# Performance work log

Measured on AMD Instinct MI355X. Metric: run time of the kernel, lower is better.

## Reference

```python
import jax, jax.numpy as jnp
import numpy as np

EMBED, NUM_CLASSES, K, BETA = 96, 3, 3, 0.75
B, H, W = 4, 512, 512
N = H * W // 16            # 16384 sampled points
N_IMP = int(BETA * N)      # 12288 importance points
N_COV = N - N_IMP          # 4096 coverage points


def point_sample(inp, points):
    """Bilinear sample inp [B,C,H,W] at points [B,N,2] in [0,1] (x,y order).
    Matches F.grid_sample(..., mode='bilinear', padding_mode='zeros', align_corners=False)
    applied to grid = 2*points - 1."""
    Bb, C, Hh, Ww = inp.shape
    g = 2.0 * points - 1.0
    ix = ((g[..., 0] + 1.0) * Ww - 1.0) / 2.0   # [B,N]
    iy = ((g[..., 1] + 1.0) * Hh - 1.0) / 2.0
    x0 = jnp.floor(ix)
    y0 = jnp.floor(iy)
    wx1 = ix - x0
    wx0 = 1.0 - wx1
    wy1 = iy - y0
    wy0 = 1.0 - wy1
    flat = inp.reshape(Bb, C, Hh * Ww)

    def corner(xc, yc, w):
        valid = (xc >= 0) & (xc < Ww) & (yc >= 0) & (yc < Hh)
        xi = jnp.clip(xc, 0, Ww - 1).astype(jnp.int32)
        yi = jnp.clip(yc, 0, Hh - 1).astype(jnp.int32)
        idx = (yi * Ww + xi)[:, None, :]                     # [B,1,N]
        v = jnp.take_along_axis(flat, idx, axis=2)           # [B,C,N]
        return v * (w * valid.astype(w.dtype))[:, None, :]

    return (corner(x0, y0, wx0 * wy0)
            + corner(x0 + 1.0, y0, wx1 * wy0)
            + corner(x0, y0 + 1.0, wx0 * wy1)
            + corner(x0 + 1.0, y0 + 1.0, wx1 * wy1))


def setup_inputs() -> dict:
    key = jax.random.key(0)
    ks = jax.random.split(key, 6)
    x = jax.random.normal(ks[0], (B, EMBED, H, W), dtype=jnp.float32)
    res = jax.random.normal(ks[1], (B, NUM_CLASSES, H, W), dtype=jnp.float32)
    out = jax.random.normal(ks[2], (B, NUM_CLASSES, H, W), dtype=jnp.float32)
    w_mlp = jax.random.normal(ks[3], (NUM_CLASSES, EMBED + NUM_CLASSES), dtype=jnp.float32) * 0.02
    over_gen = jax.random.uniform(ks[4], (B, K * N, 2), dtype=jnp.float32)
    coverage = jax.random.uniform(ks[5], (B, N_COV, 2), dtype=jnp.float32)
    return {"x": x, "res": res, "out": out, "w_mlp": w_mlp,
            "over_gen": over_gen, "coverage": coverage}


def reference(x, res, out, w_mlp, over_gen, coverage):
    # sampling_points (training branch): uncertainty from squared error map
    mask = jnp.square(out - res)                       # [B,C,H,W]
    ms = -jnp.sort(-mask, axis=1)                      # channels sorted descending
    og_map = point_sample(ms, over_gen)                # [B,C,K*N]
    uncert = og_map[:, 1] - og_map[:, 0]               # -(top1 - top2), [B,K*N]
    _, idx = jax.lax.top_k(uncert, N_IMP)              # [B,N_IMP]
    importance = jnp.take_along_axis(over_gen, idx[..., None], axis=1)  # [B,N_IMP,2]
    points = jnp.concatenate([importance, coverage], axis=1)            # [B,N,2]

    coarse = point_sample(out, points)                 # [B,C,N]
    fine = point_sample(x, points)                     # [B,EMBED,N]
    feat = jnp.concatenate([coarse, fine], axis=1)     # [B,C+EMBED,N]
    rend = jax.nn.relu(jnp.einsum('oc,bcn->bon', w_mlp, feat))  # 1x1 Conv1d, no bias
    return rend
```

## Files before the change

kernel.cpp:

```cpp
#include <hip/hip_runtime.h>
#include <stdint.h>

#define Bb    4
#define EMBED 96
#define NCH   3
#define Hh    512
#define Ww    512
#define HWSZ  (Hh * Ww)
#define KN    49152
#define NPT   16384
#define NIMP  12288
#define NCOV  4096
#define SORTN 65536
#define NBUCK 1024

__device__ __forceinline__ float opaque(float v) {
    asm volatile("" : "+v"(v));
    return v;
}

__device__ __forceinline__ void ref_coords(float p, int& i0, float& w0, float& w1) {
    float g  = 2.0f * p - 1.0f;
    float t  = (g + 1.0f) * 512.0f - 1.0f;
    float ix = t * 0.5f;
    float f  = floorf(ix);
    i0 = (int)f;
    w1 = ix - f;
    w0 = 1.0f - w1;
}

__device__ __forceinline__ uint32_t sortable_desc32(float v) {
    uint32_t u = __float_as_uint(v);
    uint32_t asc = (u >> 31) ? ~u : (u ^ 0x80000000u);
    return ~asc;
}

__device__ __forceinline__ uint32_t part1by1(uint32_t v) {
    v &= 0xFFFFu;
    v = (v | (v << 8)) & 0x00FF00FFu;
    v = (v | (v << 4)) & 0x0F0F0F0Fu;
    v = (v | (v << 2)) & 0x33333333u;
    v = (v | (v << 1)) & 0x55555555u;
    return v;
}

__global__ void build_maps(const float* __restrict__ res,
                           const float* __restrict__ outm,
                           float2* __restrict__ maps) {
    int lb  = blockIdx.y;
    int pix = blockIdx.x * blockDim.x + threadIdx.x;
    const float* r0 = res  + (size_t)lb * NCH * HWSZ;
    const float* o0 = outm + (size_t)lb * NCH * HWSZ;
    float d0 = opaque(o0[pix]            - r0[pix]);
    float d1 = opaque(o0[HWSZ + pix]     - r0[HWSZ + pix]);
    float d2 = opaque(o0[2 * HWSZ + pix] - r0[2 * HWSZ + pix]);
    float a  = opaque(d0 * d0);
    float bq = opaque(d1 * d1);
    float c  = opaque(d2 * d2);
    float m0 = fmaxf(fmaxf(a, bq), c);
    float m1 = fmaxf(fminf(a, bq), fminf(fmaxf(a, bq), c));
    maps[(size_t)lb * HWSZ + pix] = make_float2(m0, m1);
}

__global__ void uncert_keys_maps(const float2* __restrict__ maps,
                                 const float* __restrict__ over_gen,
                                 uint64_t* __restrict__ keys) {
    int lb = blockIdx.y;
    int i  = blockIdx.x * blockDim.x + threadIdx.x;
    if (i >= KN) { keys[(size_t)lb * SORTN + i] = 0xFFFFFFFFFFFFFFFFull; return; }

    float px = over_gen[((size_t)lb * KN + i) * 2 + 0];
    float py = over_gen[((size_t)lb * KN + i) * 2 + 1];
    int x0, y0;
    float wx0, wx1, wy0, wy1;
    ref_coords(px, x0, wx0, wx1);
    ref_coords(py, y0, wy0, wy1);

    const float2* mp = maps + (size_t)lb * HWSZ;
    int   cxs[4] = {x0, x0 + 1, x0, x0 + 1};
    int   cys[4] = {y0, y0, y0 + 1, y0 + 1};
    float wxs[4] = {wx0, wx1, wx0, wx1};
    float wys[4] = {wy0, wy0, wy1, wy1};

    float acc0 = 0.0f, acc1 = 0.0f;
#pragma unroll
    for (int q = 0; q < 4; ++q) {
        int xq = cxs[q], yq = cys[q];
        if (xq < 0 || xq >= Ww || yq < 0 || yq >= Hh) continue;
        float2 m = mp[yq * Ww + xq];
        float wq = opaque(wxs[q] * wys[q]);
        float t0 = opaque(wq * m.x);
        float t1 = opaque(wq * m.y);
        acc0 = opaque(acc0 + t0);
        acc1 = opaque(acc1 + t1);
    }
    float u = opaque(acc1 - acc0);
    keys[(size_t)lb * SORTN + i] =
        ((uint64_t)sortable_desc32(u) << 32) | (uint32_t)i;
}

__global__ void uncert_keys_direct(const float* __restrict__ res,
                                   const float* __restrict__ outm,
                                   const float* __restrict__ over_gen,
                                   uint64_t* __restrict__ keys) {
    int lb = blockIdx.y;
    int i  = blockIdx.x * blockDim.x + threadIdx.x;
    if (i >= KN) { keys[(size_t)lb * SORTN + i] = 0xFFFFFFFFFFFFFFFFull; return; }

    float px = over_gen[((size_t)lb * KN + i) * 2 + 0];
    float py = over_gen[((size_t)lb * KN + i) * 2 + 1];
    int x0, y0;
    float wx0, wx1, wy0, wy1;
    ref_coords(px, x0, wx0, wx1);
    ref_coords(py, y0, wy0, wy1);

    const float* r0 = res  + (size_t)lb * NCH * HWSZ;
    const float* o0 = outm + (size_t)lb * NCH * HWSZ;
    int   cxs[4] = {x0, x0 + 1, x0, x0 + 1};
    int   cys[4] = {y0, y0, y0 + 1, y0 + 1};
    float wxs[4] = {wx0, wx1, wx0, wx1};
    float wys[4] = {wy0, wy0, wy1, wy1};

    float acc0 = 0.0f, acc1 = 0.0f;
#pragma unroll
    for (int q = 0; q < 4; ++q) {
        int xq = cxs[q], yq = cys[q];
        if (xq < 0 || xq >= Ww || yq < 0 || yq >= Hh) continue;
        int off = yq * Ww + xq;
        float d0 = opaque(o0[off]            - r0[off]);
        float d1 = opaque(o0[HWSZ + off]     - r0[HWSZ + off]);
        float d2 = opaque(o0[2 * HWSZ + off] - r0[2 * HWSZ + off]);
        float a  = opaque(d0 * d0);
        float bq = opaque(d1 * d1);
        float c  = opaque(d2 * d2);
        float m0 = fmaxf(fmaxf(a, bq), c);
        float m1 = fmaxf(fminf(a, bq), fminf(fmaxf(a, bq), c));
        float wq = opaque(wxs[q] * wys[q]);
        float t0 = opaque(wq * m0);
        float t1 = opaque(wq * m1);
        acc0 = opaque(acc0 + t0);
        acc1 = opaque(acc1 + t1);
    }
    float u = opaque(acc1 - acc0);
    keys[(size_t)lb * SORTN + i] =
        ((uint64_t)sortable_desc32(u) << 32) | (uint32_t)i;
}

__global__ void __launch_bounds__(1024) bitonic_local_first(uint64_t* __restrict__ keys) {
    __shared__ uint64_t sh[2048];
    uint64_t* base = keys + (size_t)blockIdx.x * 2048;
    int t = threadIdx.x;
    sh[t]        = base[t];
    sh[t + 1024] = base[t + 1024];
    __syncthreads();
    int gbase = (blockIdx.x & 31) << 11;
    for (int k = 2; k <= 2048; k <<= 1) {
        for (int j = k >> 1; j >= 1; j >>= 1) {
            int low = t & (j - 1);
            int i = ((t ^ low) << 1) | low;
            int l = i | j;
            bool up = (((gbase + i) & k) == 0);
            uint64_t a = sh[i], c = sh[l];
            if ((a > c) == up) { sh[i] = c; sh[l] = a; }
            __syncthreads();
        }
    }
    base[t]        = sh[t];
    base[t + 1024] = sh[t + 1024];
}

__global__ void __launch_bounds__(1024) bitonic_global_fused(uint64_t* __restrict__ keys,
                                                             int m) {
    __shared__ uint64_t sh[2048];
    int lb  = blockIdx.y;
    int blk = blockIdx.x;
    int t   = threadIdx.x;
    int GS  = 1 << m;
    int GPB = 2048 >> m;
    int gstart = blk * GPB;
    int esh = 11 - m;
    uint64_t* base = keys + ((size_t)lb << 16);

    for (int s = t; s < 2048; s += 1024) {
        int e  = s >> esh;
        int gl = s & (GPB - 1);
        int g  = gstart + gl;
        int full = (g & 2047) | (e << 11) | ((g >> 11) << (11 + m));
        sh[s] = base[full];
    }
    __syncthreads();
    for (int jl = GS >> 1; jl >= 1; jl >>= 1) {
        int gl = t & (GPB - 1);
        int pe = t >> esh;
        int low = pe & (jl - 1);
        int e0 = ((pe ^ low) << 1) | low;
        int e1 = e0 | jl;
        bool up = ((((gstart + gl) >> 11) & 1) == 0);
        int s0 = e0 * GPB + gl, s1 = e1 * GPB + gl;
        uint64_t a = sh[s0], c = sh[s1];
        if ((a > c) == up) { sh[s0] = c; sh[s1] = a; }
        __syncthreads();
    }
    for (int s = t; s < 2048; s += 1024) {
        int e  = s >> esh;
        int gl = s & (GPB - 1);
        int g  = gstart + gl;
        int full = (g & 2047) | (e << 11) | ((g >> 11) << (11 + m));
        base[full] = sh[s];
    }
}

__global__ void __launch_bounds__(1024) bitonic_local_k(uint64_t* __restrict__ keys, int k) {
    __shared__ uint64_t sh[2048];
    uint64_t* base = keys + (size_t)blockIdx.x * 2048;
    int t = threadIdx.x;
    sh[t]        = base[t];
    sh[t + 1024] = base[t + 1024];
    __syncthreads();
    int gbase = (blockIdx.x & 31) << 11;
    bool up = ((gbase & k) == 0);
    for (int j = 1024; j >= 1; j >>= 1) {
        int low = t & (j - 1);
        int i = ((t ^ low) << 1) | low;
        int l = i | j;
        uint64_t a = sh[i], c = sh[l];
        if ((a > c) == up) { sh[i] = c; sh[l] = a; }
        __syncthreads();
    }
    base[t]        = sh[t];
    base[t + 1024] = sh[t + 1024];
}

static void run_sort_big(uint64_t* keys, int nb, hipStream_t stream) {
    bitonic_local_first<<<nb * 32, 1024, 0, stream>>>(keys);
    for (int kbit = 12; kbit <= 16; ++kbit) {
        bitonic_global_fused<<<dim3(32, nb), 1024, 0, stream>>>(keys, kbit - 11);
        bitonic_local_k<<<nb * 32, 1024, 0, stream>>>(keys, 1 << kbit);
    }
}

__global__ void hist_kernel(const uint64_t* __restrict__ keys,
                            const float* __restrict__ over_gen,
                            const float* __restrict__ coverage,
                            uint32_t* __restrict__ hist,
                            uint32_t* __restrict__ mort) {
    int lb = blockIdx.y;
    int n  = blockIdx.x * blockDim.x + threadIdx.x;
    float px, py;
    if (n < NIMP) {
        uint32_t idx = (uint32_t)keys[((size_t)lb << 16) + n];
        if (idx >= KN) idx = 0;
        px = over_gen[((size_t)lb * KN + idx) * 2 + 0];
        py = over_gen[((size_t)lb * KN + idx) * 2 + 1];
    } else {
        int m = n - NIMP;
        px = coverage[((size_t)lb * NCOV + m) * 2 + 0];
        py = coverage[((size_t)lb * NCOV + m) * 2 + 1];
    }
    int x0, y0;
    float w0, w1;
    ref_coords(px, x0, w0, w1);
    ref_coords(py, y0, w0, w1);
    int xi = min(max(x0, 0), Ww - 1);
    int yi = min(max(y0, 0), Hh - 1);
    uint32_t morton = part1by1((uint32_t)xi) | (part1by1((uint32_t)yi) << 1);
    uint32_t bucket = morton >> 8;
    mort[(size_t)lb * NPT + n] = bucket;
    atomicAdd(&hist[(size_t)lb * NBUCK + bucket], 1u);
}

__global__ void __launch_bounds__(1024) scan_kernel(const uint32_t* __restrict__ hist,
                                                    uint32_t* __restrict__ offs) {
    __shared__ uint32_t sh[NBUCK];
    int lb = blockIdx.x;
    int t  = threadIdx.x;
    uint32_t orig = hist[(size_t)lb * NBUCK + t];
    sh[t] = orig;
    __syncthreads();
    for (int d = 1; d < NBUCK; d <<= 1) {
        uint32_t add = (t >= d) ? sh[t - d] : 0u;
        __syncthreads();
        sh[t] += add;
        __syncthreads();
    }
    offs[(size_t)lb * NBUCK + t] = sh[t] - orig;
}

__global__ void scatter_kernel(const uint32_t* __restrict__ mort,
                               uint32_t* __restrict__ offs,
                               uint32_t* __restrict__ porder) {
    int lb = blockIdx.y;
    int n  = blockIdx.x * blockDim.x + threadIdx.x;
    uint32_t b = mort[(size_t)lb * NPT + n];
    uint32_t pos = atomicAdd(&offs[(size_t)lb * NBUCK + b], 1u);
    porder[(size_t)lb * NPT + pos] = (uint32_t)n;
}

__global__ void render_kernel(const float* __restrict__ x,
                              const float* __restrict__ outm,
                              const float* __restrict__ w_mlp,
                              const float* __restrict__ over_gen,
                              const float* __restrict__ coverage,
                              const uint64_t* __restrict__ keys,
                              const uint32_t* __restrict__ porder,
                              float* __restrict__ dst) {
    int gid = blockIdx.x * blockDim.x + threadIdx.x;
    int pt = gid >> 3, r = gid & 7;
    int lb = blockIdx.y;
    int n = pt;
    if (porder) n = porder[(size_t)lb * NPT + pt];

    float px, py;
    if (n < NIMP) {
        uint32_t idx = (uint32_t)keys[((size_t)lb << 16) + n];
        if (idx >= KN) idx = 0;
        px = over_gen[((size_t)lb * KN + idx) * 2 + 0];
        py = over_gen[((size_t)lb * KN + idx) * 2 + 1];
    } else {
        int m = n - NIMP;
        px = coverage[((size_t)lb * NCOV + m) * 2 + 0];
        py = coverage[((size_t)lb * NCOV + m) * 2 + 1];
    }

    int x0, y0;
    float wx0, wx1, wy0, wy1;
    ref_coords(px, x0, wx0, wx1);
    ref_coords(py, y0, wy0, wy1);

    int   cxs[4] = {x0, x0 + 1, x0, x0 + 1};
    int   cys[4] = {y0, y0, y0 + 1, y0 + 1};
    float wcs[4] = {wx0 * wy0, wx1 * wy0, wx0 * wy1, wx1 * wy1};
    bool  vld[4];
#pragma unroll
    for (int q = 0; q < 4; ++q)
        vld[q] = (cxs[q] >= 0) & (cxs[q] < Ww) & (cys[q] >= 0) & (cys[q] < Hh);

    float acc0 = 0.0f, acc1 = 0.0f, acc2 = 0.0f;
    for (int c = r; c < NCH + EMBED; c += 8) {
        const float* src = (c < NCH)
            ? (outm + ((size_t)lb * NCH + c) * HWSZ)
            : (x + ((size_t)lb * EMBED + (c - NCH)) * HWSZ);
        float f = 0.0f;
#pragma unroll
        for (int q = 0; q < 4; ++q) {
            if (vld[q]) f += wcs[q] * src[cys[q] * Ww + cxs[q]];
        }
        acc0 += w_mlp[c] * f;
        acc1 += w_mlp[99 + c] * f;
        acc2 += w_mlp[198 + c] * f;
    }
#pragma unroll
    for (int d = 1; d < 8; d <<= 1) {
        acc0 += __shfl_xor(acc0, d);
        acc1 += __shfl_xor(acc1, d);
        acc2 += __shfl_xor(acc2, d);
    }
    if (r == 0) {
        size_t ob = (size_t)lb * 3 * NPT + n;
        dst[ob]           = fmaxf(acc0, 0.0f);
        dst[ob + NPT]     = fmaxf(acc1, 0.0f);
        dst[ob + 2 * NPT] = fmaxf(acc2, 0.0f);
    }
}

extern "C" void kernel_launch(void* const* d_in, const int* in_sizes, int n_in,
                              void* d_out, int out_size, void* d_ws, size_t ws_size,
                              hipStream_t stream) {
    const float* x        = (const float*)d_in[0];
    const float* res      = (const float*)d_in[1];
    const float* outm     = (const float*)d_in[2];
    const float* w_mlp    = (const float*)d_in[3];
    const float* over_gen = (const float*)d_in[4];
    const float* coverage = (const float*)d_in[5];
    float* dst = (float*)d_out;

    const size_t keys_sz = (size_t)Bb * SORTN * sizeof(uint64_t);
    const size_t hist_sz = (size_t)Bb * NBUCK * sizeof(uint32_t);
    const size_t offs_sz = hist_sz;
    const size_t mort_sz = (size_t)Bb * NPT * sizeof(uint32_t);
    const size_t pord_sz = mort_sz;
    const size_t reor_sz = hist_sz + offs_sz + mort_sz + pord_sz;
    const size_t maps_sz = (size_t)Bb * HWSZ * sizeof(float2);

    uint64_t* keys = (uint64_t*)d_ws;
    dim3 gU(SORTN / 256, Bb), gP(NPT / 256, Bb), gD(NPT * 8 / 256, Bb);

    if (ws_size >= keys_sz + reor_sz + maps_sz) {
        char* pbase = (char*)d_ws + keys_sz;
        uint32_t* hist   = (uint32_t*)pbase;
        uint32_t* offs   = (uint32_t*)(pbase + hist_sz);
        uint32_t* mort   = (uint32_t*)(pbase + hist_sz + offs_sz);
        uint32_t* porder = (uint32_t*)(pbase + hist_sz + offs_sz + mort_sz);
        float2*   maps   = (float2*)(pbase + reor_sz);
        dim3 gM(HWSZ / 256, Bb);
        build_maps<<<gM, 256, 0, stream>>>(res, outm, maps);
        uncert_keys_maps<<<gU, 256, 0, stream>>>(maps, over_gen, keys);
        run_sort_big(keys, Bb, stream);
        hipMemsetAsync(hist, 0, hist_sz, stream);
        hist_kernel<<<gP, 256, 0, stream>>>(keys, over_gen, coverage, hist, mort);
        scan_kernel<<<Bb, NBUCK, 0, stream>>>(hist, offs);
        scatter_kernel<<<gP, 256, 0, stream>>>(mort, offs, porder);
        render_kernel<<<gD, 256, 0, stream>>>(x, outm, w_mlp, over_gen, coverage,
                                              keys, porder, dst);
    } else if (ws_size >= keys_sz + reor_sz) {
        char* pbase = (char*)d_ws + keys_sz;
        uint32_t* hist   = (uint32_t*)pbase;
        uint32_t* offs   = (uint32_t*)(pbase + hist_sz);
        uint32_t* mort   = (uint32_t*)(pbase + hist_sz + offs_sz);
        uint32_t* porder = (uint32_t*)(pbase + hist_sz + offs_sz + mort_sz);
        uncert_keys_direct<<<gU, 256, 0, stream>>>(res, outm, over_gen, keys);
        run_sort_big(keys, Bb, stream);
        hipMemsetAsync(hist, 0, hist_sz, stream);
        hist_kernel<<<gP, 256, 0, stream>>>(keys, over_gen, coverage, hist, mort);
        scan_kernel<<<Bb, NBUCK, 0, stream>>>(hist, offs);
        scatter_kernel<<<gP, 256, 0, stream>>>(mort, offs, porder);
        render_kernel<<<gD, 256, 0, stream>>>(x, outm, w_mlp, over_gen, coverage,
                                              keys, porder, dst);
    } else {
        uncert_keys_direct<<<gU, 256, 0, stream>>>(res, outm, over_gen, keys);
        run_sort_big(keys, Bb, stream);
        render_kernel<<<gD, 256, 0, stream>>>(x, outm, w_mlp, over_gen, coverage,
                                              keys, (const uint32_t*)nullptr, dst);
    }
}
```

Measured before the change: 283.8 us.

## Replace full bitonic sort with radix-histogram selection and compacted candidate sort

Rather than bitonic-sorting all 65536 padded keys per batch, the code builds an 11-bit histogram of key prefixes during key generation, scans it to find the cutoff bucket holding the 12288th element, and compacts candidates into a 16384-slot buffer that is then sorted. The bitonic sort also runs its inner strides (j<=64) in registers via wavefront shuffles instead of shared-memory passes with barriers. Sort work and global passes shrink, at the cost of extra kernels, atomics and memsets. If more than 16384 keys fall at or below the cutoff bucket, the excess is silently dropped, which could change the selected points.

```diff
diff --git a/kernel.cpp b/kernel.cpp
--- a/kernel.cpp
+++ b/kernel.cpp
@@ -11,7 +11,8 @@
 #define NPT   16384
 #define NIMP  12288
 #define NCOV  4096
-#define SORTN 65536
+#define SELB  2048
+#define CSEG  16384
 #define NBUCK 1024
 
 __device__ __forceinline__ float opaque(float v) {
@@ -42,6 +43,38 @@
     v = (v | (v << 2)) & 0x33333333u;
     v = (v | (v << 1)) & 0x55555555u;
     return v;
+}
+
+__device__ __forceinline__ uint64_t shfl64(uint64_t v, int lanexor) {
+    int2 p;
+    p.x = (int)(v & 0xFFFFFFFFull);
+    p.y = (int)(v >> 32);
+    p.x = __shfl_xor(p.x, lanexor);
+    p.y = __shfl_xor(p.y, lanexor);
+    return ((uint64_t)(uint32_t)p.y << 32) | (uint32_t)p.x;
+}
+
+__device__ __forceinline__ void ce_shfl(uint64_t& v, int idx, int j, int k) {
+    uint64_t o = shfl64(v, j);
+    bool low = (idx & j) == 0;
+    bool up  = (idx & k) == 0;
+    uint64_t mn = (v < o) ? v : o;
+    uint64_t mx = (v < o) ? o : v;
+    v = (low == up) ? mn : mx;
+}
+
+__device__ __forceinline__ void ce_reg(uint64_t& a, uint64_t& b, bool up) {
+    uint64_t mn = (a < b) ? a : b;
+    uint64_t mx = (a < b) ? b : a;
+    a = up ? mn : mx;
+    b = up ? mx : mn;
+}
+
+__device__ __forceinline__ void reg_tail(uint64_t& a, uint64_t& b, int ia, int ib, int k) {
+    bool up = (ia & k) == 0;
+    ce_reg(a, b, up);
+#pragma unroll
+    for (int j = 32; j >= 1; j >>= 1) { ce_shfl(a, ia, j, k); ce_shfl(b, ib, j, k); }
 }
 
 __global__ void build_maps(const float* __restrict__ res,
@@ -64,10 +97,10 @@
 
 __global__ void uncert_keys_maps(const float2* __restrict__ maps,
                                  const float* __restrict__ over_gen,
-                                 uint64_t* __restrict__ keys) {
+                                 uint64_t* __restrict__ keys,
+                                 uint32_t* __restrict__ hist) {
     int lb = blockIdx.y;
     int i  = blockIdx.x * blockDim.x + threadIdx.x;
-    if (i >= KN) { keys[(size_t)lb * SORTN + i] = 0xFFFFFFFFFFFFFFFFull; return; }
 
     float px = over_gen[((size_t)lb * KN + i) * 2 + 0];
     float py = over_gen[((size_t)lb * KN + i) * 2 + 1];
@@ -95,17 +128,18 @@
         acc1 = opaque(acc1 + t1);
     }
     float u = opaque(acc1 - acc0);
-    keys[(size_t)lb * SORTN + i] =
-        ((uint64_t)sortable_desc32(u) << 32) | (uint32_t)i;
+    uint64_t key = ((uint64_t)sortable_desc32(u) << 32) | (uint32_t)i;
+    keys[(size_t)lb * KN + i] = key;
+    atomicAdd(&hist[(size_t)lb * SELB + (uint32_t)(key >> 53)], 1u);
 }
 
 __global__ void uncert_keys_direct(const float* __restrict__ res,
                                    const float* __restrict__ outm,
                                    const float* __restrict__ over_gen,
-                                   uint64_t* __restrict__ keys) {
+                                   uint64_t* __restrict__ keys,
+                                   uint32_t* __restrict__ hist) {
     int lb = blockIdx.y;
     int i  = blockIdx.x * blockDim.x + threadIdx.x;
-    if (i >= KN) { keys[(size_t)lb * SORTN + i] = 0xFFFFFFFFFFFFFFFFull; return; }
 
     float px = over_gen[((size_t)lb * KN + i) * 2 + 0];
     float py = over_gen[((size_t)lb * KN + i) * 2 + 1];
@@ -142,35 +176,80 @@
         acc1 = opaque(acc1 + t1);
     }
     float u = opaque(acc1 - acc0);
-    keys[(size_t)lb * SORTN + i] =
-        ((uint64_t)sortable_desc32(u) << 32) | (uint32_t)i;
-}
-
-__global__ void __launch_bounds__(1024) bitonic_local_first(uint64_t* __restrict__ keys) {
+    uint64_t key = ((uint64_t)sortable_desc32(u) << 32) | (uint32_t)i;
+    keys[(size_t)lb * KN + i] = key;
+    atomicAdd(&hist[(size_t)lb * SELB + (uint32_t)(key >> 53)], 1u);
+}
+
+__global__ void __launch_bounds__(1024) scan_findC(const uint32_t* __restrict__ hist,
+                                                   uint32_t* __restrict__ cutC) {
+    __shared__ uint32_t s[1024];
+    int lb = blockIdx.x, t = threadIdx.x;
+    uint32_t h0 = hist[(size_t)lb * SELB + 2 * t];
+    uint32_t h1 = hist[(size_t)lb * SELB + 2 * t + 1];
+    s[t] = h0 + h1;
+    __syncthreads();
+    for (int d = 1; d < 1024; d <<= 1) {
+        uint32_t add = (t >= d) ? s[t - d] : 0u;
+        __syncthreads();
+        s[t] += add;
+        __syncthreads();
+    }
+    uint32_t incl = s[t];
+    uint32_t excl = incl - h0 - h1;
+    if (excl < NIMP && excl + h0 >= NIMP) cutC[lb] = 2 * t;
+    uint32_t p1 = excl + h0;
+    if (p1 < NIMP && incl >= NIMP) cutC[lb] = 2 * t + 1;
+}
+
+__global__ void compact_kernel(const uint64_t* __restrict__ keys,
+                               const uint32_t* __restrict__ cutC,
+                               uint32_t* __restrict__ ccnt,
+                               uint64_t* __restrict__ cbuf) {
+    int lb = blockIdx.y;
+    int i  = blockIdx.x * blockDim.x + threadIdx.x;
+    uint64_t key = keys[(size_t)lb * KN + i];
+    uint32_t b = (uint32_t)(key >> 53);
+    if (b <= cutC[lb]) {
+        uint32_t pos = atomicAdd(&ccnt[lb], 1u);
+        if (pos < CSEG) cbuf[(size_t)lb * CSEG + pos] = key;
+    }
+}
+
+__global__ void __launch_bounds__(1024) bl_first_s(uint64_t* __restrict__ keys,
+                                                   int tile_mask) {
     __shared__ uint64_t sh[2048];
     uint64_t* base = keys + (size_t)blockIdx.x * 2048;
     int t = threadIdx.x;
-    sh[t]        = base[t];
-    sh[t + 1024] = base[t + 1024];
-    __syncthreads();
-    int gbase = (blockIdx.x & 31) << 11;
-    for (int k = 2; k <= 2048; k <<= 1) {
-        for (int j = k >> 1; j >= 1; j >>= 1) {
+    int l = t & 63, w = t >> 6;
+    int ea = (w << 7) + l, eb = ea + 64;
+    int gbase = (blockIdx.x & tile_mask) << 11;
+    int ia = gbase + ea, ib = gbase + eb;
+    uint64_t a = base[ea], b = base[eb];
+    for (int k = 2; k <= 64; k <<= 1)
+        for (int j = k >> 1; j >= 1; j >>= 1) { ce_shfl(a, ia, j, k); ce_shfl(b, ib, j, k); }
+    reg_tail(a, b, ia, ib, 128);
+    for (int k = 256; k <= 2048; k <<= 1) {
+        sh[ea] = a; sh[eb] = b;
+        __syncthreads();
+        for (int j = k >> 1; j >= 128; j >>= 1) {
             int low = t & (j - 1);
-            int i = ((t ^ low) << 1) | low;
-            int l = i | j;
-            bool up = (((gbase + i) & k) == 0);
-            uint64_t a = sh[i], c = sh[l];
-            if ((a > c) == up) { sh[i] = c; sh[l] = a; }
+            int i0 = ((t ^ low) << 1) | low;
+            int i1 = i0 | j;
+            bool up = (((gbase + i0) & k) == 0);
+            uint64_t A = sh[i0], C = sh[i1];
+            if ((A > C) == up) { sh[i0] = C; sh[i1] = A; }
             __syncthreads();
         }
-    }
-    base[t]        = sh[t];
-    base[t + 1024] = sh[t + 1024];
-}
-
-__global__ void __launch_bounds__(1024) bitonic_global_fused(uint64_t* __restrict__ keys,
-                                                             int m) {
+        a = sh[ea]; b = sh[eb];
+        __syncthreads();
+        reg_tail(a, b, ia, ib, k);
+    }
+    base[ea] = a; base[eb] = b;
+}
+
+__global__ void __launch_bounds__(1024) fused_global(uint64_t* __restrict__ keys,
+                                                     int m, int seg) {
     __shared__ uint64_t sh[2048];
     int lb  = blockIdx.y;
     int blk = blockIdx.x;
@@ -179,7 +258,7 @@
     int GPB = 2048 >> m;
     int gstart = blk * GPB;
     int esh = 11 - m;
-    uint64_t* base = keys + ((size_t)lb << 16);
+    uint64_t* base = keys + (size_t)lb * seg;
 
     for (int s = t; s < 2048; s += 1024) {
         int e  = s >> esh;
@@ -197,8 +276,8 @@
         int e1 = e0 | jl;
         bool up = ((((gstart + gl) >> 11) & 1) == 0);
         int s0 = e0 * GPB + gl, s1 = e1 * GPB + gl;
-        uint64_t a = sh[s0], c = sh[s1];
-        if ((a > c) == up) { sh[s0] = c; sh[s1] = a; }
+        uint64_t A = sh[s0], C = sh[s1];
+        if ((A > C) == up) { sh[s0] = C; sh[s1] = A; }
         __syncthreads();
     }
     for (int s = t; s < 2048; s += 1024) {
@@ -210,45 +289,50 @@
     }
 }
 
-__global__ void __launch_bounds__(1024) bitonic_local_k(uint64_t* __restrict__ keys, int k) {
+__global__ void __launch_bounds__(1024) bl_k_s(uint64_t* __restrict__ keys,
+                                               int k, int tile_mask) {
     __shared__ uint64_t sh[2048];
     uint64_t* base = keys + (size_t)blockIdx.x * 2048;
     int t = threadIdx.x;
-    sh[t]        = base[t];
-    sh[t + 1024] = base[t + 1024];
+    int l = t & 63, w = t >> 6;
+    int ea = (w << 7) + l, eb = ea + 64;
+    int gbase = (blockIdx.x & tile_mask) << 11;
+    int ia = gbase + ea, ib = gbase + eb;
+    bool up = ((gbase & k) == 0);
+    sh[t] = base[t]; sh[t + 1024] = base[t + 1024];
     __syncthreads();
-    int gbase = (blockIdx.x & 31) << 11;
-    bool up = ((gbase & k) == 0);
-    for (int j = 1024; j >= 1; j >>= 1) {
+    for (int j = 1024; j >= 128; j >>= 1) {
         int low = t & (j - 1);
-        int i = ((t ^ low) << 1) | low;
-        int l = i | j;
-        uint64_t a = sh[i], c = sh[l];
-        if ((a > c) == up) { sh[i] = c; sh[l] = a; }
-        __syncthreads();
-    }
-    base[t]        = sh[t];
-    base[t + 1024] = sh[t + 1024];
-}
-
-static void run_sort_big(uint64_t* keys, int nb, hipStream_t stream) {
-    bitonic_local_first<<<nb * 32, 1024, 0, stream>>>(keys);
-    for (int kbit = 12; kbit <= 16; ++kbit) {
-        bitonic_global_fused<<<dim3(32, nb), 1024, 0, stream>>>(keys, kbit - 11);
-        bitonic_local_k<<<nb * 32, 1024, 0, stream>>>(keys, 1 << kbit);
-    }
-}
-
-__global__ void hist_kernel(const uint64_t* __restrict__ keys,
+        int i0 = ((t ^ low) << 1) | low;
+        int i1 = i0 | j;
+        uint64_t A = sh[i0], C = sh[i1];
+        if ((A > C) == up) { sh[i0] = C; sh[i1] = A; }
+        __syncthreads();
+    }
+    uint64_t a = sh[ea], b = sh[eb];
+    reg_tail(a, b, ia, ib, k);
+    base[ea] = a; base[eb] = b;
+}
+
+static void run_sort_c(uint64_t* cbuf, int nb, hipStream_t stream) {
+    const int tiles = CSEG / 2048;
+    bl_first_s<<<nb * tiles, 1024, 0, stream>>>(cbuf, tiles - 1);
+    for (int kbit = 12; kbit <= 14; ++kbit) {
+        fused_global<<<dim3(tiles, nb), 1024, 0, stream>>>(cbuf, kbit - 11, CSEG);
+        bl_k_s<<<nb * tiles, 1024, 0, stream>>>(cbuf, 1 << kbit, tiles - 1);
+    }
+}
+
+__global__ void hist_kernel(const uint64_t* __restrict__ cbuf,
                             const float* __restrict__ over_gen,
                             const float* __restrict__ coverage,
-                            uint32_t* __restrict__ hist,
+                            uint32_t* __restrict__ histP,
                             uint32_t* __restrict__ mort) {
     int lb = blockIdx.y;
     int n  = blockIdx.x * blockDim.x + threadIdx.x;
     float px, py;
     if (n < NIMP) {
-        uint32_t idx = (uint32_t)keys[((size_t)lb << 16) + n];
+        uint32_t idx = (uint32_t)cbuf[(size_t)lb * CSEG + n];
         if (idx >= KN) idx = 0;
         px = over_gen[((size_t)lb * KN + idx) * 2 + 0];
         py = over_gen[((size_t)lb * KN + idx) * 2 + 1];
@@ -266,15 +350,15 @@
     uint32_t morton = part1by1((uint32_t)xi) | (part1by1((uint32_t)yi) << 1);
     uint32_t bucket = morton >> 8;
     mort[(size_t)lb * NPT + n] = bucket;
-    atomicAdd(&hist[(size_t)lb * NBUCK + bucket], 1u);
-}
-
-__global__ void __launch_bounds__(1024) scan_kernel(const uint32_t* __restrict__ hist,
-                                                    uint32_t* __restrict__ offs) {
+    atomicAdd(&histP[(size_t)lb * NBUCK + bucket], 1u);
+}
+
+__global__ void __launch_bounds__(1024) scan_kernel(const uint32_t* __restrict__ histP,
+                                                    uint32_t* __restrict__ offsP) {
     __shared__ uint32_t sh[NBUCK];
     int lb = blockIdx.x;
     int t  = threadIdx.x;
-    uint32_t orig = hist[(size_t)lb * NBUCK + t];
+    uint32_t orig = histP[(size_t)lb * NBUCK + t];
     sh[t] = orig;
     __syncthreads();
     for (int d = 1; d < NBUCK; d <<= 1) {
@@ -283,16 +367,16 @@
         sh[t] += add;
         __syncthreads();
     }
-    offs[(size_t)lb * NBUCK + t] = sh[t] - orig;
+    offsP[(size_t)lb * NBUCK + t] = sh[t] - orig;
 }
 
 __global__ void scatter_kernel(const uint32_t* __restrict__ mort,
-                               uint32_t* __restrict__ offs,
+                               uint32_t* __restrict__ offsP,
                                uint32_t* __restrict__ porder) {
     int lb = blockIdx.y;
     int n  = blockIdx.x * blockDim.x + threadIdx.x;
     uint32_t b = mort[(size_t)lb * NPT + n];
-    uint32_t pos = atomicAdd(&offs[(size_t)lb * NBUCK + b], 1u);
+    uint32_t pos = atomicAdd(&offsP[(size_t)lb * NBUCK + b], 1u);
     porder[(size_t)lb * NPT + pos] = (uint32_t)n;
 }
 
@@ -301,18 +385,17 @@
                               const float* __restrict__ w_mlp,
                               const float* __restrict__ over_gen,
                               const float* __restrict__ coverage,
-                              const uint64_t* __restrict__ keys,
+                              const uint64_t* __restrict__ cbuf,
                               const uint32_t* __restrict__ porder,
                               float* __restrict__ dst) {
     int gid = blockIdx.x * blockDim.x + threadIdx.x;
     int pt = gid >> 3, r = gid & 7;
     int lb = blockIdx.y;
-    int n = pt;
-    if (porder) n = porder[(size_t)lb * NPT + pt];
+    int n = porder[(size_t)lb * NPT + pt];
 
     float px, py;
     if (n < NIMP) {
-        uint32_t idx = (uint32_t)keys[((size_t)lb << 16) + n];
+        uint32_t idx = (uint32_t)cbuf[(size_t)lb * CSEG + n];
         if (idx >= KN) idx = 0;
         px = over_gen[((size_t)lb * KN + idx) * 2 + 0];
         py = over_gen[((size_t)lb * KN + idx) * 2 + 1];
@@ -374,52 +457,50 @@
     const float* coverage = (const float*)d_in[5];
     float* dst = (float*)d_out;
 
-    const size_t keys_sz = (size_t)Bb * SORTN * sizeof(uint64_t);
-    const size_t hist_sz = (size_t)Bb * NBUCK * sizeof(uint32_t);
-    const size_t offs_sz = hist_sz;
+    const size_t cbuf_sz = (size_t)Bb * CSEG * sizeof(uint64_t);
+    const size_t keys_sz = (size_t)Bb * KN * sizeof(uint64_t);
+    const size_t hist_sz = (size_t)Bb * SELB * sizeof(uint32_t);
+    const size_t cnt_sz  = 64;
+    const size_t cut_sz  = 64;
+    const size_t hP_sz   = (size_t)Bb * NBUCK * sizeof(uint32_t);
+    const size_t oP_sz   = hP_sz;
+    const size_t zero_sz = hist_sz + cnt_sz + cut_sz + hP_sz;
     const size_t mort_sz = (size_t)Bb * NPT * sizeof(uint32_t);
     const size_t pord_sz = mort_sz;
-    const size_t reor_sz = hist_sz + offs_sz + mort_sz + pord_sz;
+    const size_t base_sz = cbuf_sz + keys_sz + zero_sz + oP_sz + mort_sz + pord_sz;
     const size_t maps_sz = (size_t)Bb * HWSZ * sizeof(float2);
 
-    uint64_t* keys = (uint64_t*)d_ws;
-    dim3 gU(SORTN / 256, Bb), gP(NPT / 256, Bb), gD(NPT * 8 / 256, Bb);
-
-    if (ws_size >= keys_sz + reor_sz + maps_sz) {
-        char* pbase = (char*)d_ws + keys_sz;
-        uint32_t* hist   = (uint32_t*)pbase;
-        uint32_t* offs   = (uint32_t*)(pbase + hist_sz);
-        uint32_t* mort   = (uint32_t*)(pbase + hist_sz + offs_sz);
-        uint32_t* porder = (uint32_t*)(pbase + hist_sz + offs_sz + mort_sz);
-        float2*   maps   = (float2*)(pbase + reor_sz);
+    char* p = (char*)d_ws;
+    uint64_t* cbuf   = (uint64_t*)p;                 p += cbuf_sz;
+    uint64_t* keys   = (uint64_t*)p;                 p += keys_sz;
+    char*     zbase  = p;
+    uint32_t* hist   = (uint32_t*)p;                 p += hist_sz;
+    uint32_t* ccnt   = (uint32_t*)p;                 p += cnt_sz;
+    uint32_t* cutC   = (uint32_t*)p;                 p += cut_sz;
+    uint32_t* histP  = (uint32_t*)p;                 p += hP_sz;
+    uint32_t* offsP  = (uint32_t*)p;                 p += oP_sz;
+    uint32_t* mort   = (uint32_t*)p;                 p += mort_sz;
+    uint32_t* porder = (uint32_t*)p;                 p += pord_sz;
+    float2*   maps   = (float2*)p;
+
+    dim3 gK(KN / 256, Bb), gP(NPT / 256, Bb), gD(NPT * 8 / 256, Bb);
+
+    hipMemsetAsync(zbase, 0, zero_sz, stream);
+    hipMemsetAsync(cbuf, 0xFF, cbuf_sz, stream);
+
+    if (ws_size >= base_sz + maps_sz) {
         dim3 gM(HWSZ / 256, Bb);
         build_maps<<<gM, 256, 0, stream>>>(res, outm, maps);
-        uncert_keys_maps<<<gU, 256, 0, stream>>>(maps, over_gen, keys);
-        run_sort_big(keys, Bb, stream);
-        hipMemsetAsync(hist, 0, hist_sz, stream);
-        hist_kernel<<<gP, 256, 0, stream>>>(keys, over_gen, coverage, hist, mort);
-        scan_kernel<<<Bb, NBUCK, 0, stream>>>(hist, offs);
-        scatter_kernel<<<gP, 256, 0, stream>>>(mort, offs, porder);
-        render_kernel<<<gD, 256, 0, stream>>>(x, outm, w_mlp, over_gen, coverage,
-                                              keys, porder, dst);
-    } else if (ws_size >= keys_sz + reor_sz) {
-        char* pbase = (char*)d_ws + keys_sz;
-        uint32_t* hist   = (uint32_t*)pbase;
-        uint32_t* offs   = (uint32_t*)(pbase + hist_sz);
-        uint32_t* mort   = (uint32_t*)(pbase + hist_sz + offs_sz);
-        uint32_t* porder = (uint32_t*)(pbase + hist_sz + offs_sz + mort_sz);
-        uncert_keys_direct<<<gU, 256, 0, stream>>>(res, outm, over_gen, keys);
-        run_sort_big(keys, Bb, stream);
-        hipMemsetAsync(hist, 0, hist_sz, stream);
-        hist_kernel<<<gP, 256, 0, stream>>>(keys, over_gen, coverage, hist, mort);
-        scan_kernel<<<Bb, NBUCK, 0, stream>>>(hist, offs);
-        scatter_kernel<<<gP, 256, 0, stream>>>(mort, offs, porder);
-        render_kernel<<<gD, 256, 0, stream>>>(x, outm, w_mlp, over_gen, coverage,
-                                              keys, porder, dst);
+        uncert_keys_maps<<<gK, 256, 0, stream>>>(maps, over_gen, keys, hist);
     } else {
-        uncert_keys_direct<<<gU, 256, 0, stream>>>(res, outm, over_gen, keys);
-        run_sort_big(keys, Bb, stream);
-        render_kernel<<<gD, 256, 0, stream>>>(x, outm, w_mlp, over_gen, coverage,
-                                              keys, (const uint32_t*)nullptr, dst);
-    }
-}
+        uncert_keys_direct<<<gK, 256, 0, stream>>>(res, outm, over_gen, keys, hist);
+    }
+    scan_findC<<<Bb, 1024, 0, stream>>>(hist, cutC);
+    compact_kernel<<<gK, 256, 0, stream>>>(keys, cutC, ccnt, cbuf);
+    run_sort_c(cbuf, Bb, stream);
+    hist_kernel<<<gP, 256, 0, stream>>>(cbuf, over_gen, coverage, histP, mort);
+    scan_kernel<<<Bb, NBUCK, 0, stream>>>(histP, offsP);
+    scatter_kernel<<<gP, 256, 0, stream>>>(mort, offsP, porder);
+    render_kernel<<<gD, 256, 0, stream>>>(x, outm, w_mlp, over_gen, coverage,
+                                          cbuf, porder, dst);
+}
```

Measured after the change: 416.8 us. +46.9%, slower.
